# Performance work log

Measured on AMD Instinct MI355X. Metric: run time of the kernel, lower is better.

The kernel has to match this reference:

```python
import jax, jax.numpy as jnp
from jax import lax
import numpy as np

B, L, A = 4096, 168, 128   # batch, attn_length, attn_size
FN, FS = 32, 1             # filter_num, filter_size
FD = A - FS + 1            # feature_dim


def setup_inputs() -> dict:
    key = jax.random.key(0)
    ks = jax.random.split(key, 5)
    return {
        "query": jax.random.normal(ks[0], (B, 2 * A), jnp.float32),
        "attn_states": jax.random.normal(ks[1], (B, L, A), jnp.float32),
        "W_q": jax.random.normal(ks[2], (2 * A, FN), jnp.float32) / np.sqrt(2 * A),
        "conv_k": jax.random.normal(ks[3], (L, FS, 1, FN), jnp.float32) / np.sqrt(L * FS),
        "conv_b": jnp.zeros((FN,), jnp.float32),
        "W_out": jax.random.normal(ks[4], (2 * A + FN, A), jnp.float32) / np.sqrt(2 * A + FN),
        "b_out": jnp.zeros((A,), jnp.float32),
    }


def reference(query, attn_states, W_q, conv_k, conv_b, W_out, b_out):
    # w: [B, FN] -- Dense(filter_num, no bias)(query)
    w = query @ W_q
    # Conv2D over [B, L, A, 1] with kernel [L, FS] 'VALID' -> [B, 1, FD, FN]
    x = attn_states[..., None]
    cv = lax.conv_general_dilated(
        x, conv_k, window_strides=(1, 1), padding='VALID',
        dimension_numbers=('NHWC', 'HWIO', 'NHWC')) + conv_b
    cv = cv[:, 0]                                   # [B, FD, FN]
    # sigmoid-gated attention score over filter dim
    s = jnp.einsum('bfk,bk->bf', cv, w)             # [B, FD]
    a = jax.nn.sigmoid(s)
    d = jnp.einsum('bf,bfk->bk', a, cv)             # [B, FN]
    new_attns = jnp.concatenate([query, d], axis=1) @ W_out + b_out  # [B, A]
    new_attn_states = attn_states[:, 1:, :]         # [B, L-1, A]
    return new_attns, new_attn_states
```

## Files before the change

kernel.cpp:

```cpp
#include <hip/hip_runtime.h>
#include <math.h>

#define BB  4096
#define LL  168
#define AA  128
#define FNN 32

__global__ __launch_bounds__(256, 4)
void tpa_fused(const float* __restrict__ query,
               const float* __restrict__ attn_states,
               const float* __restrict__ W_q,
               const float* __restrict__ conv_k,
               const float* __restrict__ conv_b,
               const float* __restrict__ W_out,
               const float* __restrict__ b_out,
               float* __restrict__ out_attns,
               float* __restrict__ out_states)
{
    const int b    = blockIdx.x;
    const int t    = threadIdx.x;
    const int lane = t & 63;
    const int w    = __builtin_amdgcn_readfirstlane(t >> 6);

    __shared__ float qrow[256];
    __shared__ float red[512];
    __shared__ float sh_wv[32];
    __shared__ float sh_a[128];
    __shared__ float sh_d[32];

    qrow[t] = query[(size_t)b * 256 + t];
    __syncthreads();

    {
        const int n = t & 31, kc = t >> 5;
        float p = 0.f;
        #pragma unroll
        for (int i = 0; i < 32; ++i) {
            const int k = (kc << 5) + i;
            p += qrow[k] * W_q[k * FNN + n];
        }
        red[t] = p;
    }
    __syncthreads();
    if (t < 32) {
        float s = 0.f;
        #pragma unroll
        for (int kc = 0; kc < 8; ++kc) s += red[(kc << 5) + t];
        sh_wv[t] = s;
    }
    __syncthreads();

    float cv0[8], cv1[8];
    #pragma unroll
    for (int j = 0; j < 8; ++j) { cv0[j] = 0.f; cv1[j] = 0.f; }

    const float* asp = attn_states + (size_t)b * LL * AA + lane * 2;
    float*       osp = out_states  + (size_t)b * (LL - 1) * AA + lane * 2;
    const float* kp  = conv_k + w * 8;

    #pragma unroll 4
    for (int l = 0; l < LL; ++l) {
        const float2 av = *(const float2*)(asp + (size_t)l * AA);
        const float4 ka = *(const float4*)(kp + l * FNN);
        const float4 kb = *(const float4*)(kp + l * FNN + 4);
        const float kk[8] = {ka.x, ka.y, ka.z, ka.w, kb.x, kb.y, kb.z, kb.w};
        #pragma unroll
        for (int j = 0; j < 8; ++j) {
            cv0[j] += av.x * kk[j];
            cv1[j] += av.y * kk[j];
        }
        if (((l & 3) == w) && (l > 0)) {
            *(float2*)(osp + (size_t)(l - 1) * AA) = av;
        }
    }

    #pragma unroll
    for (int j = 0; j < 8; ++j) {
        const float cb = conv_b[w * 8 + j];
        cv0[j] += cb;
        cv1[j] += cb;
    }

    float wv[8];
    #pragma unroll
    for (int j = 0; j < 8; ++j) wv[j] = sh_wv[w * 8 + j];
    float sp0 = 0.f, sp1 = 0.f;
    #pragma unroll
    for (int j = 0; j < 8; ++j) { sp0 += cv0[j] * wv[j]; sp1 += cv1[j] * wv[j]; }
    red[(lane * 2 + 0) * 4 + w] = sp0;
    red[(lane * 2 + 1) * 4 + w] = sp1;
    __syncthreads();
    if (t < 128) {
        const float s = red[t * 4] + red[t * 4 + 1] + red[t * 4 + 2] + red[t * 4 + 3];
        sh_a[t] = 1.f / (1.f + expf(-s));
    }
    __syncthreads();

    const float a0 = sh_a[lane * 2], a1 = sh_a[lane * 2 + 1];
    float dp[8];
    #pragma unroll
    for (int j = 0; j < 8; ++j) dp[j] = a0 * cv0[j] + a1 * cv1[j];
    #pragma unroll
    for (int off = 32; off > 0; off >>= 1) {
        #pragma unroll
        for (int j = 0; j < 8; ++j) dp[j] += __shfl_xor(dp[j], off);
    }
    if (lane == 0) {
        #pragma unroll
        for (int j = 0; j < 8; ++j) sh_d[w * 8 + j] = dp[j];
    }
    __syncthreads();

    {
        const int m = t & 127, half = t >> 7;
        float acc = 0.f;
        const int kbase = half << 7;
        for (int k = kbase; k < kbase + 128; ++k)
            acc += qrow[k] * W_out[k * AA + m];
        if (half) {
            #pragma unroll
            for (int j = 0; j < 32; ++j)
                acc += sh_d[j] * W_out[(256 + j) * AA + m];
        } else {
            acc += b_out[m];
        }
        red[t] = acc;
    }
    __syncthreads();
    if (t < 128)
        out_attns[(size_t)b * AA + t] = red[t] + red[t + 128];
}

extern "C" void kernel_launch(void* const* d_in, const int* in_sizes, int n_in,
                              void* d_out, int out_size, void* d_ws, size_t ws_size,
                              hipStream_t stream) {
    const float* query       = (const float*)d_in[0];
    const float* attn_states = (const float*)d_in[1];
    const float* W_q         = (const float*)d_in[2];
    const float* conv_k      = (const float*)d_in[3];
    const float* conv_b      = (const float*)d_in[4];
    const float* W_out       = (const float*)d_in[5];
    const float* b_out       = (const float*)d_in[6];

    float* out_attns  = (float*)d_out;
    float* out_states = (float*)d_out + (size_t)BB * AA;

    tpa_fused<<<BB, 256, 0, stream>>>(query, attn_states, W_q, conv_k, conv_b,
                                      W_out, b_out, out_attns, out_states);
}
```

Before: 693.2 us.

## Split conv rows by parity and filters by half across waves, with prefetch

Re-partitions the per-batch conv work. Each wave now covers 16 filters over every other row, instead of 8 filters over all 168 rows, so each attn_states row is read by two waves rather than four. Partial convolution results are combined through the existing score reduction and an extra shared-memory sum for d. The row loop is software-pipelined with explicit double-buffered loads, and conv kernel weights are loaded as 16-wide vectors. In exchange, each thread holds more live registers (32 accumulators plus the vector loads), and the kernel adds one more block barrier.

```diff
diff --git a/kernel.cpp b/kernel.cpp
--- a/kernel.cpp
+++ b/kernel.cpp
@@ -5,6 +5,8 @@
 #define LL  168
 #define AA  128
 #define FNN 32
+
+typedef float f16v __attribute__((ext_vector_type(16)));
 
 __global__ __launch_bounds__(256, 4)
 void tpa_fused(const float* __restrict__ query,
@@ -20,12 +22,15 @@
     const int b    = blockIdx.x;
     const int t    = threadIdx.x;
     const int lane = t & 63;
-    const int w    = __builtin_amdgcn_readfirstlane(t >> 6);
+    const int wid  = __builtin_amdgcn_readfirstlane(t >> 6);
+    const int h    = wid & 1;
+    const int p    = wid >> 1;
 
     __shared__ float qrow[256];
     __shared__ float red[512];
     __shared__ float sh_wv[32];
     __shared__ float sh_a[128];
+    __shared__ float sh_dp[64];
     __shared__ float sh_d[32];
 
     qrow[t] = query[(size_t)b * 256 + t];
@@ -33,13 +38,13 @@
 
     {
         const int n = t & 31, kc = t >> 5;
-        float p = 0.f;
+        float pp = 0.f;
         #pragma unroll
         for (int i = 0; i < 32; ++i) {
             const int k = (kc << 5) + i;
-            p += qrow[k] * W_q[k * FNN + n];
+            pp += qrow[k] * W_q[k * FNN + n];
         }
-        red[t] = p;
+        red[t] = pp;
     }
     __syncthreads();
     if (t < 32) {
@@ -50,45 +55,65 @@
     }
     __syncthreads();
 
-    float cv0[8], cv1[8];
+    float wvv[16];
     #pragma unroll
-    for (int j = 0; j < 8; ++j) { cv0[j] = 0.f; cv1[j] = 0.f; }
+    for (int n = 0; n < 16; ++n) wvv[n] = sh_wv[h * 16 + n];
 
-    const float* asp = attn_states + (size_t)b * LL * AA + lane * 2;
-    float*       osp = out_states  + (size_t)b * (LL - 1) * AA + lane * 2;
-    const float* kp  = conv_k + w * 8;
+    float cv0[16], cv1[16];
+    #pragma unroll
+    for (int n = 0; n < 16; ++n) { cv0[n] = 0.f; cv1[n] = 0.f; }
 
-    #pragma unroll 4
-    for (int l = 0; l < LL; ++l) {
-        const float2 av = *(const float2*)(asp + (size_t)l * AA);
-        const float4 ka = *(const float4*)(kp + l * FNN);
-        const float4 kb = *(const float4*)(kp + l * FNN + 4);
-        const float kk[8] = {ka.x, ka.y, ka.z, ka.w, kb.x, kb.y, kb.z, kb.w};
+    const float* asp = attn_states + (size_t)b * (LL * AA) + p * AA + lane * 2;
+    float*       osp = out_states  + (size_t)b * ((LL - 1) * AA) + lane * 2;
+    const float* kwp = conv_k + h * 16;
+    const bool dostore = (h == 0);
+
+    float2 a_cur = *(const float2*)asp;
+    f16v   k_cur = *(const f16v*)(kwp + p * FNN);
+    float2 a_nxt;
+    f16v   k_nxt;
+
+    for (int i = 0; i < 84; i += 2) {
+        a_nxt = *(const float2*)(asp + (size_t)(i + 1) * 256);
+        k_nxt = *(const f16v*)(kwp + (size_t)(2 * (i + 1) + p) * FNN);
+        if (dostore) {
+            const int ro = 2 * i + p - 1;
+            if (ro >= 0) *(float2*)(osp + (size_t)ro * AA) = a_cur;
+        }
         #pragma unroll
-        for (int j = 0; j < 8; ++j) {
-            cv0[j] += av.x * kk[j];
-            cv1[j] += av.y * kk[j];
+        for (int n = 0; n < 16; ++n) {
+            cv0[n] += a_cur.x * k_cur[n];
+            cv1[n] += a_cur.y * k_cur[n];
         }
-        if (((l & 3) == w) && (l > 0)) {
-            *(float2*)(osp + (size_t)(l - 1) * AA) = av;
+        if (i + 2 < 84) {
+            a_cur = *(const float2*)(asp + (size_t)(i + 2) * 256);
+            k_cur = *(const f16v*)(kwp + (size_t)(2 * (i + 2) + p) * FNN);
+        }
+        if (dostore) {
+            const int ro = 2 * i + 1 + p;
+            *(float2*)(osp + (size_t)ro * AA) = a_nxt;
+        }
+        #pragma unroll
+        for (int n = 0; n < 16; ++n) {
+            cv0[n] += a_nxt.x * k_nxt[n];
+            cv1[n] += a_nxt.y * k_nxt[n];
         }
     }
 
-    #pragma unroll
-    for (int j = 0; j < 8; ++j) {
-        const float cb = conv_b[w * 8 + j];
-        cv0[j] += cb;
-        cv1[j] += cb;
+    if (p == 0) {
+        #pragma unroll
+        for (int n = 0; n < 16; ++n) {
+            const float cb = conv_b[h * 16 + n];
+            cv0[n] += cb;
+            cv1[n] += cb;
+        }
     }
 
-    float wv[8];
-    #pragma unroll
-    for (int j = 0; j < 8; ++j) wv[j] = sh_wv[w * 8 + j];
     float sp0 = 0.f, sp1 = 0.f;
     #pragma unroll
-    for (int j = 0; j < 8; ++j) { sp0 += cv0[j] * wv[j]; sp1 += cv1[j] * wv[j]; }
-    red[(lane * 2 + 0) * 4 + w] = sp0;
-    red[(lane * 2 + 1) * 4 + w] = sp1;
+    for (int n = 0; n < 16; ++n) { sp0 += cv0[n] * wvv[n]; sp1 += cv1[n] * wvv[n]; }
+    red[(lane * 2 + 0) * 4 + wid] = sp0;
+    red[(lane * 2 + 1) * 4 + wid] = sp1;
     __syncthreads();
     if (t < 128) {
         const float s = red[t * 4] + red[t * 4 + 1] + red[t * 4 + 2] + red[t * 4 + 3];
@@ -97,27 +122,30 @@
     __syncthreads();
 
     const float a0 = sh_a[lane * 2], a1 = sh_a[lane * 2 + 1];
-    float dp[8];
+    float dp[16];
     #pragma unroll
-    for (int j = 0; j < 8; ++j) dp[j] = a0 * cv0[j] + a1 * cv1[j];
+    for (int n = 0; n < 16; ++n) dp[n] = a0 * cv0[n] + a1 * cv1[n];
     #pragma unroll
     for (int off = 32; off > 0; off >>= 1) {
         #pragma unroll
-        for (int j = 0; j < 8; ++j) dp[j] += __shfl_xor(dp[j], off);
+        for (int n = 0; n < 16; ++n) dp[n] += __shfl_xor(dp[n], off);
     }
     if (lane == 0) {
         #pragma unroll
-        for (int j = 0; j < 8; ++j) sh_d[w * 8 + j] = dp[j];
+        for (int n = 0; n < 16; ++n) sh_dp[wid * 16 + n] = dp[n];
     }
+    __syncthreads();
+    if (t < 32) sh_d[t] = sh_dp[t] + sh_dp[t + 32];
     __syncthreads();
 
     {
-        const int m = t & 127, half = t >> 7;
+        const int m = t & 127, khalf = t >> 7;
         float acc = 0.f;
-        const int kbase = half << 7;
+        const int kbase = khalf << 7;
+        #pragma unroll 4
         for (int k = kbase; k < kbase + 128; ++k)
             acc += qrow[k] * W_out[k * AA + m];
-        if (half) {
+        if (khalf) {
             #pragma unroll
             for (int j = 0; j < 32; ++j)
                 acc += sh_d[j] * W_out[(256 + j) * AA + m];
```

After: 666.3 us. 3.9% less time.
